# Kernel optimization log

Hardware: AMD Instinct MI355X
Metric: run time of the kernel (lower is better)

## Reference

```python
import jax, jax.numpy as jnp
import numpy as np

B, C, H, W = 16, 768, 32, 32
HEADS = 12
EPS = 1e-5


def _make_rel_index(h, w):
    coords = np.stack(np.meshgrid(np.arange(h), np.arange(w), indexing='ij'))  # [2,h,w]
    cf = coords.reshape(2, -1)                      # [2,N]
    rel = cf[:, :, None] - cf[:, None, :]           # [2,N,N]
    rel = rel.transpose(1, 2, 0).copy()             # [N,N,2]
    rel[:, :, 0] += h - 1
    rel[:, :, 1] += w - 1
    rel[:, :, 0] *= 2 * w - 1
    return jnp.asarray(rel.sum(-1), dtype=jnp.int32)  # [N,N]


def setup_inputs() -> dict:
    key = jax.random.key(0)
    ks = jax.random.split(key, 8)
    s = 0.02
    return {
        'x': jax.random.normal(ks[0], (B, C, H, W), jnp.float32),
        'rpb_table': jax.random.normal(ks[1], ((2 * H - 1) * (2 * W - 1), HEADS), jnp.float32) * s,
        'g1': jnp.ones((C,), jnp.float32),
        'b1': jnp.zeros((C,), jnp.float32),
        'q_w': jax.random.normal(ks[2], (C, C), jnp.float32) * s,
        'q_b': jnp.zeros((C,), jnp.float32),
        'kv_w': jax.random.normal(ks[3], (2 * C, C), jnp.float32) * s,
        'kv_b': jnp.zeros((2 * C,), jnp.float32),
        'proj_w': jax.random.normal(ks[4], (C, C), jnp.float32) * s,
        'proj_b': jnp.zeros((C,), jnp.float32),
        'g2': jnp.ones((C,), jnp.float32),
        'b2': jnp.zeros((C,), jnp.float32),
        'fc1_w': jax.random.normal(ks[5], (4 * C, C), jnp.float32) * s,
        'fc1_b': jnp.zeros((4 * C,), jnp.float32),
        'fc2_w': jax.random.normal(ks[6], (C, 4 * C), jnp.float32) * s,
        'fc2_b': jnp.zeros((C,), jnp.float32),
        'rel_index': _make_rel_index(H, W),
    }


def _ln(t, g, b):
    m = t.mean(-1, keepdims=True)
    v = ((t - m) ** 2).mean(-1, keepdims=True)
    return (t - m) * jax.lax.rsqrt(v + EPS) * g + b


def reference(x, rpb_table, g1, b1, q_w, q_b, kv_w, kv_b, proj_w, proj_b,
              g2, b2, fc1_w, fc1_b, fc2_w, fc2_b, rel_index):
    b, c, h, w = x.shape
    n = h * w
    heads = rpb_table.shape[1]
    hd = c // heads
    scale = hd ** -0.5

    xt = x.reshape(b, c, n).transpose(0, 2, 1)  # [B,N,C]

    # --- attention branch ---
    xn = _ln(xt, g1, b1)
    q = (xn @ q_w.T + q_b).reshape(b, n, heads, hd).transpose(0, 2, 1, 3)  # [B,h,N,d]
    kv = (xn @ kv_w.T + kv_b).reshape(b, n, 2, heads, hd)
    k = kv[:, :, 0].transpose(0, 2, 1, 3)  # [B,h,N,d]
    v = kv[:, :, 1].transpose(0, 2, 1, 3)  # [B,h,N,d]
    attn = jnp.einsum('bhnd,bhmd->bhnm', q, k) * scale  # [B,h,N,N]
    bias = rpb_table[rel_index].transpose(2, 0, 1)      # [h,N,N]
    attn = jax.nn.softmax(attn + bias[None], axis=-1)
    o = jnp.einsum('bhnm,bhmd->bhnd', attn, v).transpose(0, 2, 1, 3).reshape(b, n, c)
    o = o @ proj_w.T + proj_b
    xt = xt + o

    # --- mlp branch ---
    xn = _ln(xt, g2, b2)
    h1 = jax.nn.gelu(xn @ fc1_w.T + fc1_b, approximate=False)
    xt = xt + (h1 @ fc2_w.T + fc2_b)

    return xt.transpose(0, 2, 1).reshape(b, c, h, w)
```

## Files before the change

### kernel.cpp

```cpp
#include <hip/hip_runtime.h>
#include <hip/hip_bf16.h>
#include <math.h>

typedef unsigned short u16;
typedef unsigned int u32;
typedef float f32x4 __attribute__((ext_vector_type(4)));
typedef short bf16x8 __attribute__((ext_vector_type(8)));
typedef unsigned short us4 __attribute__((ext_vector_type(4)));
typedef int i32x4 __attribute__((ext_vector_type(4)));

struct alignas(16) F4 { float v[4]; };
template <int N> struct Tag { static constexpr int v = N; };

static constexpr int Bb = 16;
static constexpr int Cc = 768;
static constexpr int Nn = 1024;
static constexpr int NH = 12;
static constexpr int HD = 64;
static constexpr float LOG2E = 1.4426950408889634f;

static __device__ __forceinline__ u16 f2bf(float f) {
  union { float f; unsigned u; } v; v.f = f;
  unsigned u = v.u;
  u += 0x7fffu + ((u >> 16) & 1u);
  return (u16)(u >> 16);
}
static __device__ __forceinline__ float bf2f(u16 x) {
  union { unsigned u; float f; } v; v.u = ((unsigned)x) << 16; return v.f;
}
static __device__ __forceinline__ void gload16(const u16* g, u16* l) {
  __builtin_amdgcn_global_load_lds((const __attribute__((address_space(1))) u32*)g,
                                   (__attribute__((address_space(3))) u32*)l, 16, 0, 0);
}
static __device__ __forceinline__ float gelu_f(float v) {
  float z = v * 0.70710678118654752f;
  float az = fabsf(z);
  float t = __builtin_amdgcn_rcpf(1.f + 0.3275911f * az);
  float poly = t * (0.254829592f + t * (-0.284496736f + t * (1.421413741f +
               t * (-1.453152027f + t * 1.061405429f))));
  float e = __builtin_amdgcn_exp2f(-az * az * LOG2E);
  float erfv = 1.f - poly * e;
  erfv = (z < 0.f) ? -erfv : erfv;
  return 0.5f * v * (1.f + erfv);
}
static __device__ __forceinline__ us4 pack4(const float* s) {
  us4 r;
  r[0] = f2bf(s[0]); r[1] = f2bf(s[1]); r[2] = f2bf(s[2]); r[3] = f2bf(s[3]);
  return r;
}

__global__ __launch_bounds__(256) void k_pre_all(const float* __restrict__ q_w,
    const float* __restrict__ kv_w, const float* __restrict__ proj_w,
    const float* __restrict__ fc1_w, const float* __restrict__ fc2_w,
    const float* __restrict__ q_b, const float* __restrict__ kv_b,
    u16* __restrict__ wqkv, u16* __restrict__ wproj, u16* __restrict__ wfc1,
    u16* __restrict__ wfc2, float* __restrict__ bqkv,
    const float* __restrict__ x, u16* __restrict__ xt,
    const float* __restrict__ rpb, const int* __restrict__ rel,
    u16* __restrict__ bias2) {
  const int bid = blockIdx.x, tid = threadIdx.x;
  if (bid < 6913) {
    int i4 = bid * 256 + tid;
    if (i4 >= 1769664) return;
    int i = i4 * 4;
    if (i < 589824) {
      f32x4 sv = *(const f32x4*)&q_w[i];
      *(us4*)&wqkv[i] = pack4((const float*)&sv);
    } else if (i < 1769472) {
      f32x4 sv = *(const f32x4*)&kv_w[i - 589824];
      *(us4*)&wqkv[i] = pack4((const float*)&sv);
    } else if (i < 2359296) {
      f32x4 sv = *(const f32x4*)&proj_w[i - 1769472];
      *(us4*)&wproj[i - 1769472] = pack4((const float*)&sv);
    } else if (i < 4718592) {
      f32x4 sv = *(const f32x4*)&fc1_w[i - 2359296];
      *(us4*)&wfc1[i - 2359296] = pack4((const float*)&sv);
    } else if (i < 7077888) {
      f32x4 sv = *(const f32x4*)&fc2_w[i - 4718592];
      *(us4*)&wfc2[i - 4718592] = pack4((const float*)&sv);
    } else if (i < 7078656) {
      f32x4 sv;
      if (i - 7077888 < 768) sv = *(const f32x4*)&q_b[i - 7077888];
      else                   sv = *(const f32x4*)&kv_b[i - 7078656];
      *(f32x4*)&bqkv[i - 7077888] = sv;
    } else {
      f32x4 sv = *(const f32x4*)&kv_b[i - 7078656];
      *(f32x4*)&bqkv[i - 7077888] = sv;
    }
  } else if (bid < 19201) {
    __shared__ float tile[32][33];
    int j = bid - 6913;
    int n0 = (j & 31) * 32, c0 = ((j >> 5) % 24) * 32, b = j / 768;
    int tx = tid & 31, ty = tid >> 5;
    const float* xp = x + (size_t)b * Cc * Nn;
    #pragma unroll
    for (int i = 0; i < 32; i += 8)
      tile[ty + i][tx] = xp[(size_t)(c0 + ty + i) * Nn + n0 + tx];
    __syncthreads();
    u16* xtp = xt + (size_t)b * Nn * Cc;
    #pragma unroll
    for (int i = 0; i < 32; i += 8)
      xtp[(size_t)(n0 + ty + i) * Cc + c0 + tx] = f2bf(tile[tx][ty + i]);
  } else {
    int idx = (bid - 19201) * 256 + tid;
    int kg = idx & 255, q = (idx >> 8) & 1023, h = idx >> 18;
    int k = kg * 4;
    i32x4 rv = *(const i32x4*)&rel[(size_t)q * Nn + k];
    us4 ov;
    ov[0] = f2bf(rpb[rv[0] * NH + h] * LOG2E);
    ov[1] = f2bf(rpb[rv[1] * NH + h] * LOG2E);
    ov[2] = f2bf(rpb[rv[2] * NH + h] * LOG2E);
    ov[3] = f2bf(rpb[rv[3] * NH + h] * LOG2E);
    *(us4*)&bias2[((size_t)h * Nn + q) * Nn + k] = ov;
  }
}

__global__ __launch_bounds__(256) void k_layernorm(const u16* __restrict__ in,
    const float* __restrict__ gam, const float* __restrict__ bet,
    u16* __restrict__ out) {
  int wave = threadIdx.x >> 6, lane = threadIdx.x & 63;
  int row = blockIdx.x * 4 + wave;
  const u16* p = in + (size_t)row * Cc;
  float v[12]; float s = 0.f;
  #pragma unroll
  for (int i = 0; i < 6; i++) {
    u32 pr = *(const u32*)&p[2 * (lane + i * 64)];
    v[2 * i]     = bf2f((u16)(pr & 0xffff));
    v[2 * i + 1] = bf2f((u16)(pr >> 16));
    s += v[2 * i] + v[2 * i + 1];
  }
  #pragma unroll
  for (int m = 32; m >= 1; m >>= 1) s += __shfl_xor(s, m);
  float mean = s * (1.f / 768.f);
  float q = 0.f;
  #pragma unroll
  for (int i = 0; i < 12; i++) { float d = v[i] - mean; q += d * d; }
  #pragma unroll
  for (int m = 32; m >= 1; m >>= 1) q += __shfl_xor(q, m);
  float rstd = rsqrtf(q * (1.f / 768.f) + 1e-5f);
  u16* o = out + (size_t)row * Cc;
  #pragma unroll
  for (int i = 0; i < 6; i++) {
    int j = 2 * (lane + i * 64);
    u16 lo = f2bf((v[2 * i]     - mean) * rstd * gam[j]     + bet[j]);
    u16 hi = f2bf((v[2 * i + 1] - mean) * rstd * gam[j + 1] + bet[j + 1]);
    *(u32*)&o[j] = (u32)lo | ((u32)hi << 16);
  }
}

struct GemmArgs {
  const u16* A; const u16* W; const float* bias;
  int M, N, K;
  const u16* resBf;
  float* outF;
  u16* outBf;
  u16 *q, *k, *v;
};

template <int EPI>
__global__ __launch_bounds__(512, 2) void k_gemm(GemmArgs p) {
  extern __shared__ f32x4 smv[];
  u16* lA = (u16*)smv;
  u16* lB = (u16*)smv + 2 * 256 * 64;
  const int tid = threadIdx.x;
  const int wave = tid >> 6, lane = tid & 63;
  const int l15 = lane & 15, g = lane >> 4, h7 = l15 & 7;
  const int wr = wave >> 2, wc = wave & 3;
  const int rl = tid >> 3, cc8 = tid & 7;
  const int nwg = gridDim.x * gridDim.y;
  const int wg = blockIdx.y * gridDim.x + blockIdx.x;
  const int swz = (wg & 7) * (nwg >> 3) + (wg >> 3);
  const int bn = (swz % gridDim.x) * 256, bm = (swz / gridDim.x) * 256;
  const int K = p.K;

  f32x4 acc[8][4];
  #pragma unroll
  for (int i = 0; i < 8; i++)
    #pragma unroll
    for (int j = 0; j < 4; j++) acc[i][j] = (f32x4){0.f, 0.f, 0.f, 0.f};

  const u16* Ab = p.A + (size_t)bm * K;
  const u16* Wb = p.W + (size_t)bn * K;
  const int csw = (cc8 ^ (rl & 7)) * 8;

  auto stageA = [&](int buf, int k0, int half) {
    int r0 = half * 64 + rl, r1 = r0 + 128;
    gload16(Ab + (size_t)r0 * K + k0 + csw, &lA[buf * 16384 + r0 * 64 + cc8 * 8]);
    gload16(Ab + (size_t)r1 * K + k0 + csw, &lA[buf * 16384 + r1 * 64 + cc8 * 8]);
  };
  auto stageB = [&](int buf, int k0, int half) {
    int r0 = ((rl >> 5) << 6) + half * 32 + (rl & 31), r1 = r0 + 128;
    gload16(Wb + (size_t)r0 * K + k0 + csw, &lB[buf * 16384 + r0 * 64 + cc8 * 8]);
    gload16(Wb + (size_t)r1 * K + k0 + csw, &lB[buf * 16384 + r1 * 64 + cc8 * 8]);
  };

  bf16x8 a[4][2], bq[4][2];
  auto rdA = [&](int buf, int mt, int kk) {
    int row = wr * 128 + mt * 16 + l15;
    return *(const bf16x8*)&lA[buf * 16384 + row * 64 + (((kk << 2) + g) ^ h7) * 8];
  };
  auto rdB = [&](int buf, int nt, int kk) {
    int row = wc * 64 + nt * 16 + l15;
    return *(const bf16x8*)&lB[buf * 16384 + row * 64 + (((kk << 2) + g) ^ h7) * 8];
  };
  auto MF = [&](auto MBt, auto NBt) {
    constexpr int MB = decltype(MBt)::v, NB = decltype(NBt)::v;
    __builtin_amdgcn_s_setprio(1);
    #pragma unroll
    for (int kk = 0; kk < 2; kk++)
      #pragma unroll
      for (int mi = 0; mi < 4; mi++)
        #pragma unroll
        for (int ni = 0; ni < 2; ni++)
          acc[MB + mi][NB + ni] = __builtin_amdgcn_mfma_f32_16x16x32_bf16(
              a[mi][kk], bq[NB + ni][kk], acc[MB + mi][NB + ni], 0, 0, 0);
    __builtin_amdgcn_s_setprio(0);
  };

  stageA(0, 0, 0); stageB(0, 0, 0); stageB(0, 0, 1); stageA(0, 0, 1);
  stageA(1, 64, 0);
  asm volatile("s_waitcnt vmcnt(6)" ::: "memory");
  __builtin_amdgcn_s_barrier();

  auto TILE = [&](int t, auto tag) {
    constexpr int TAIL = decltype(tag)::v;
    const int buf = t & 1, nb = buf ^ 1;
    const int k1 = (t + 1) * 64;
    #pragma unroll
    for (int mi = 0; mi < 4; mi++) { a[mi][0] = rdA(buf, mi, 0); a[mi][1] = rdA(buf, mi, 1); }
    #pragma unroll
    for (int ni = 0; ni < 2; ni++) { bq[ni][0] = rdB(buf, ni, 0); bq[ni][1] = rdB(buf, ni, 1); }
    if constexpr (TAIL < 2) {
      stageB(nb, k1, 0);
      asm volatile("s_waitcnt vmcnt(6)" ::: "memory");
    } else {
      asm volatile("s_waitcnt vmcnt(2)" ::: "memory");
    }
    __builtin_amdgcn_s_barrier();
    __builtin_amdgcn_sched_barrier(0);
    MF(Tag<0>{}, Tag<0>{});
    #pragma unroll
    for (int ni = 0; ni < 2; ni++) { bq[2 + ni][0] = rdB(buf, 2 + ni, 0); bq[2 + ni][1] = rdB(buf, 2 + ni, 1); }
    if constexpr (TAIL < 2) {
      stageB(nb, k1, 1);
      asm volatile("s_waitcnt vmcnt(6)" ::: "memory");
    } else {
      asm volatile("s_waitcnt vmcnt(0)" ::: "memory");
    }
    __builtin_amdgcn_s_barrier();
    __builtin_amdgcn_sched_barrier(0);
    MF(Tag<0>{}, Tag<2>{});
    #pragma unroll
    for (int mi = 0; mi < 4; mi++) { a[mi][0] = rdA(buf, 4 + mi, 0); a[mi][1] = rdA(buf, 4 + mi, 1); }
    if constexpr (TAIL < 2) stageA(nb, k1, 1);
    __builtin_amdgcn_s_barrier();
    __builtin_amdgcn_sched_barrier(0);
    MF(Tag<4>{}, Tag<2>{});
    if constexpr (TAIL == 0) {
      stageA(buf, k1 + 64, 0);
      asm volatile("s_waitcnt vmcnt(6)" ::: "memory");
    } else if constexpr (TAIL == 1) {
      asm volatile("s_waitcnt vmcnt(4)" ::: "memory");
    }
    __builtin_amdgcn_s_barrier();
    __builtin_amdgcn_sched_barrier(0);
    MF(Tag<4>{}, Tag<0>{});
  };

  const int NT = K >> 6;
  for (int t = 0; t < NT - 2; ++t) TILE(t, Tag<0>{});
  TILE(NT - 2, Tag<1>{});
  TILE(NT - 1, Tag<2>{});

  #pragma unroll
  for (int mt = 0; mt < 8; mt++) {
    int rowb = bm + wr * 128 + mt * 16 + g * 4;
    #pragma unroll
    for (int nt = 0; nt < 4; nt++) {
      int col = bn + wc * 64 + nt * 16 + l15;
      float bias = p.bias[col];
      if constexpr (EPI == 0) {
        #pragma unroll
        for (int r = 0; r < 4; r++) {
          int grow = rowb + r;
          int bb = grow >> 10, nnq = grow & 1023;
          float val = acc[mt][nt][r] + bias;
          if (col < 768) {
            int head = col >> 6, d = col & 63;
            p.q[(((size_t)bb * NH + head) * Nn + nnq) * HD + d] = f2bf(val * (0.125f * LOG2E));
          } else {
            int j2 = col - 768;
            if (j2 < 768) {
              int head = j2 >> 6, d = j2 & 63;
              p.k[(((size_t)bb * NH + head) * Nn + nnq) * HD + d] = f2bf(val);
            } else {
              int j3 = j2 - 768;
              int head = j3 >> 6, d = j3 & 63;
              p.v[(((size_t)bb * NH + head) * HD + d) * Nn + nnq] = f2bf(val);
            }
          }
        }
      } else if constexpr (EPI == 1) {
        #pragma unroll
        for (int r = 0; r < 4; r++) {
          size_t idx = (size_t)(rowb + r) * p.N + col;
          p.outBf[idx] = f2bf(acc[mt][nt][r] + bias + bf2f(p.resBf[idx]));
        }
      } else if constexpr (EPI == 2) {
        #pragma unroll
        for (int r = 0; r < 4; r++) {
          float val = acc[mt][nt][r] + bias;
          p.outBf[(size_t)(rowb + r) * p.N + col] = f2bf(gelu_f(val));
        }
      } else {
        int bb = rowb >> 10, n0 = rowb & 1023;
        F4 ov;
        #pragma unroll
        for (int r = 0; r < 4; r++)
          ov.v[r] = acc[mt][nt][r] + bias + bf2f(p.resBf[(size_t)(rowb + r) * Cc + col]);
        *(F4*)&p.outF[((size_t)bb * Cc + col) * Nn + n0] = ov;
      }
    }
  }
}

__global__ __launch_bounds__(512, 4) void k_attn(const u16* __restrict__ qt,
    const u16* __restrict__ kt_, const u16* __restrict__ vtt,
    const u16* __restrict__ bias2, u16* __restrict__ o) {
  __shared__ __align__(16) u16 lK[3][64 * 64];
  __shared__ __align__(16) u16 lV[3][64 * 64];
  __shared__ __align__(16) u16 lP[8][16 * 64];
  const int tid = threadIdx.x, wave = tid >> 6, lane = tid & 63;
  const int l15 = lane & 15, g = lane >> 4;
  const int i_ = blockIdx.x;
  const int slot = i_ >> 3;
  const int hx = (i_ & 7) * 12 + (slot >> 4);
  const int b = slot & 15, h = hx >> 3;
  const int q0 = (hx & 7) * 128 + wave * 16;
  const size_t bh  = ((size_t)b * NH + h) * Nn * HD;
  const size_t bhT = ((size_t)b * NH + h) * HD * Nn;
  const u16* biasH = bias2 + (size_t)h * Nn * Nn;
  u16* myP = &lP[wave][0];
  const float THR = 8.f * LOG2E;
  const int sRow = tid >> 3, sCol = tid & 7;
  const int h7 = l15 & 7;

  bf16x8 qa0, qa1;
  {
    const u16* qp = qt + bh + (size_t)(q0 + l15) * HD + g * 8;
    qa0 = *(const bf16x8*)qp;
    qa1 = *(const bf16x8*)(qp + 32);
  }
  bf16x8 ones;
  #pragma unroll
  for (int i = 0; i < 8; i++) ones[i] = (short)0x3F80;

  f32x4 ao[4];
  f32x4 al;
  float mr = -1e30f;
  #pragma unroll
  for (int d = 0; d < 4; d++) ao[d] = (f32x4){0.f, 0.f, 0.f, 0.f};
  al = (f32x4){0.f, 0.f, 0.f, 0.f};

  auto issueKV = [&](int kt0, int buf) {
    int cs = (sCol ^ (sRow & 7)) << 3;
    gload16(kt_ + bh + (size_t)(kt0 + sRow) * HD + cs, &lK[buf][sRow * 64 + sCol * 8]);
    gload16(vtt + bhT + (size_t)sRow * Nn + kt0 + cs, &lV[buf][sRow * 64 + sCol * 8]);
  };

  issueKV(0, 0);
  issueKV(64, 1);
  int buf = 0, nbuf = 2;
  for (int t = 0; t < 16; ++t) {
    if (t < 15) asm volatile("s_waitcnt vmcnt(2) lgkmcnt(0)" ::: "memory");
    else        asm volatile("s_waitcnt vmcnt(0) lgkmcnt(0)" ::: "memory");
    __builtin_amdgcn_s_barrier();
    __builtin_amdgcn_sched_barrier(0);

    us4 bvv[4];
    #pragma unroll
    for (int nt = 0; nt < 4; nt++)
      bvv[nt] = *(const us4*)(biasH + (size_t)(q0 + l15) * Nn + t * 64 + nt * 16 + g * 4);
    __builtin_amdgcn_sched_barrier(0);
    if (t < 14) issueKV((t + 2) * 64, nbuf);
    __builtin_amdgcn_sched_barrier(0);

    f32x4 s[4];
    __builtin_amdgcn_s_setprio(1);
    #pragma unroll
    for (int nt = 0; nt < 4; nt++) {
      const int row = nt * 16 + l15;
      bf16x8 kb0 = *(const bf16x8*)&lK[buf][row * 64 + ((g ^ h7) << 3)];
      bf16x8 kb1 = *(const bf16x8*)&lK[buf][row * 64 + (((g + 4) ^ h7) << 3)];
      s[nt] = __builtin_amdgcn_mfma_f32_16x16x32_bf16(kb0, qa0,
                (f32x4){0.f, 0.f, 0.f, 0.f}, 0, 0, 0);
      s[nt] = __builtin_amdgcn_mfma_f32_16x16x32_bf16(kb1, qa1, s[nt], 0, 0, 0);
    }
    __builtin_amdgcn_s_setprio(0);

    #pragma unroll
    for (int nt = 0; nt < 4; nt++) {
      #pragma unroll
      for (int r = 0; r < 4; r++) s[nt][r] += bf2f(bvv[nt][r]);
    }
    float pm = fmaxf(fmaxf(s[0][0], s[0][1]), fmaxf(s[0][2], s[0][3]));
    #pragma unroll
    for (int nt = 1; nt < 4; nt++)
      pm = fmaxf(pm, fmaxf(fmaxf(s[nt][0], s[nt][1]), fmaxf(s[nt][2], s[nt][3])));
    pm = fmaxf(pm, __shfl_xor(pm, 16));
    pm = fmaxf(pm, __shfl_xor(pm, 32));
    if (__any(pm > mr + THR)) {
      float mnew = fmaxf(mr, pm);
      float fac = __builtin_amdgcn_exp2f(mr - mnew);
      mr = mnew;
      f32x4 facO;
      #pragma unroll
      for (int r = 0; r < 4; r++) facO[r] = __shfl(fac, g * 4 + r);
      #pragma unroll
      for (int d = 0; d < 4; d++) ao[d] *= facO;
      al *= facO;
    }
    #pragma unroll
    for (int nt = 0; nt < 4; nt++) {
      #pragma unroll
      for (int r = 0; r < 4; r++)
        s[nt][r] = __builtin_amdgcn_exp2f(s[nt][r] - mr);
    }
    #pragma unroll
    for (int nt = 0; nt < 4; nt++) {
      u32 w0, w1;
      asm("v_cvt_pk_bf16_f32 %0, %1, %2" : "=v"(w0) : "v"(s[nt][0]), "v"(s[nt][1]));
      asm("v_cvt_pk_bf16_f32 %0, %1, %2" : "=v"(w1) : "v"(s[nt][2]), "v"(s[nt][3]));
      int cbase = (((2 * nt + (g >> 1)) ^ h7) << 3) + (g & 1) * 4;
      *(u32*)&myP[l15 * 64 + cbase]     = w0;
      *(u32*)&myP[l15 * 64 + cbase + 2] = w1;
    }
    __builtin_amdgcn_s_setprio(1);
    #pragma unroll
    for (int kc = 0; kc < 2; kc++) {
      bf16x8 pa = *(const bf16x8*)&myP[l15 * 64 + (((4 * kc + g) ^ h7) << 3)];
      al = __builtin_amdgcn_mfma_f32_16x16x32_bf16(pa, ones, al, 0, 0, 0);
      #pragma unroll
      for (int d = 0; d < 4; d++) {
        const int rv = d * 16 + l15;
        bf16x8 vb = *(const bf16x8*)&lV[buf][rv * 64 + (((kc * 4 + g) ^ h7) << 3)];
        ao[d] = __builtin_amdgcn_mfma_f32_16x16x32_bf16(pa, vb, ao[d], 0, 0, 0);
      }
    }
    __builtin_amdgcn_s_setprio(0);
    buf = (buf == 2) ? 0 : buf + 1;
    nbuf = (nbuf == 2) ? 0 : nbuf + 1;
  }
  f32x4 linv;
  #pragma unroll
  for (int r = 0; r < 4; r++) linv[r] = __builtin_amdgcn_rcpf(al[r]);
  #pragma unroll
  for (int r = 0; r < 4; r++) {
    int qg = q0 + g * 4 + r;
    u16* op = o + ((size_t)b * Nn + qg) * Cc + h * HD;
    #pragma unroll
    for (int d = 0; d < 4; d++)
      op[d * 16 + l15] = f2bf(ao[d][r] * linv[r]);
  }
}

extern "C" void kernel_launch(void* const* d_in, const int* in_sizes, int n_in,
                              void* d_out, int out_size, void* d_ws, size_t ws_size,
                              hipStream_t stream) {
  const float* x      = (const float*)d_in[0];
  const float* rpb    = (const float*)d_in[1];
  const float* g1     = (const float*)d_in[2];
  const float* b1v    = (const float*)d_in[3];
  const float* q_w    = (const float*)d_in[4];
  const float* q_b    = (const float*)d_in[5];
  const float* kv_w   = (const float*)d_in[6];
  const float* kv_b   = (const float*)d_in[7];
  const float* proj_w = (const float*)d_in[8];
  const float* proj_b = (const float*)d_in[9];
  const float* g2     = (const float*)d_in[10];
  const float* b2v    = (const float*)d_in[11];
  const float* fc1_w  = (const float*)d_in[12];
  const float* fc1_b  = (const float*)d_in[13];
  const float* fc2_w  = (const float*)d_in[14];
  const float* fc2_b  = (const float*)d_in[15];
  const int*   rel    = (const int*)d_in[16];
  float* out = (float*)d_out;

  char* ws = (char*)d_ws;
  size_t off = 0;
  auto alloc = [&](size_t bytes) -> void* {
    void* p = ws + off;
    off += (bytes + 255) & ~(size_t)255;
    return p;
  };
  u16*   wqkv  = (u16*)alloc((size_t)2304 * 768 * 2);
  u16*   wproj = (u16*)alloc((size_t)768 * 768 * 2);
  u16*   wfc1  = (u16*)alloc((size_t)3072 * 768 * 2);
  u16*   wfc2  = (u16*)alloc((size_t)768 * 3072 * 2);
  float* bqkv  = (float*)alloc((size_t)2304 * 4);
  u16*   xt    = (u16*)alloc((size_t)16384 * 768 * 2);
  u16*   xt2   = (u16*)alloc((size_t)16384 * 768 * 2);
  u16*   xn    = (u16*)alloc((size_t)16384 * 768 * 2);
  u16*   qb_   = (u16*)alloc((size_t)Bb * NH * Nn * HD * 2);
  u16*   kb_   = (u16*)alloc((size_t)Bb * NH * Nn * HD * 2);
  u16*   vb_   = (u16*)alloc((size_t)Bb * NH * Nn * HD * 2);
  u16*   ob_   = (u16*)alloc((size_t)16384 * 768 * 2);
  u16*   h1    = qb_;
  u16*   bias2 = xt2;

  hipFuncSetAttribute((const void*)k_gemm<0>, hipFuncAttributeMaxDynamicSharedMemorySize, 131072);
  hipFuncSetAttribute((const void*)k_gemm<1>, hipFuncAttributeMaxDynamicSharedMemorySize, 131072);
  hipFuncSetAttribute((const void*)k_gemm<2>, hipFuncAttributeMaxDynamicSharedMemorySize, 131072);
  hipFuncSetAttribute((const void*)k_gemm<3>, hipFuncAttributeMaxDynamicSharedMemorySize, 131072);

  k_pre_all<<<31489, 256, 0, stream>>>(q_w, kv_w, proj_w, fc1_w, fc2_w, q_b, kv_b,
                                       wqkv, wproj, wfc1, wfc2, bqkv,
                                       x, xt, rpb, rel, bias2);

  k_layernorm<<<4096, 256, 0, stream>>>(xt, g1, b1v, xn);

  GemmArgs ga = {};
  ga.A = xn; ga.W = wqkv; ga.bias = bqkv; ga.M = 16384; ga.N = 2304; ga.K = 768;
  ga.q = qb_; ga.k = kb_; ga.v = vb_;
  k_gemm<0><<<dim3(9, 64), 512, 131072, stream>>>(ga);

  k_attn<<<1536, 512, 0, stream>>>(qb_, kb_, vb_, bias2, ob_);

  GemmArgs gp = {};
  gp.A = ob_; gp.W = wproj; gp.bias = proj_b; gp.M = 16384; gp.N = 768; gp.K = 768;
  gp.resBf = xt; gp.outBf = xt2;
  k_gemm<1><<<dim3(3, 64), 512, 131072, stream>>>(gp);

  k_layernorm<<<4096, 256, 0, stream>>>(xt2, g2, b2v, xn);

  GemmArgs gf1 = {};
  gf1.A = xn; gf1.W = wfc1; gf1.bias = fc1_b; gf1.M = 16384; gf1.N = 3072; gf1.K = 768;
  gf1.outBf = h1;
  k_gemm<2><<<dim3(12, 64), 512, 131072, stream>>>(gf1);

  GemmArgs gf2 = {};
  gf2.A = h1; gf2.W = wfc2; gf2.bias = fc2_b; gf2.M = 16384; gf2.N = 768; gf2.K = 3072;
  gf2.resBf = xt2; gf2.outF = out;
  k_gemm<3><<<dim3(3, 64), 512, 131072, stream>>>(gf2);
}
```

Before: 491.4 us.

## Use smaller 128x128 tile GEMM kernel for N=768 projection and fc2

Adds a new GEMM kernel with 128x128 tiles, 256 threads and static shared memory, and uses it for the proj and fc2 GEMMs whose N=768 gave only 192 workgroups with the large-tile kernel. The goal is to raise the workgroup count to 768 so all compute units get work and waves are better balanced. The new kernel has no multi-stage pipelining: it does a single-buffered K loop with synchronizations around direct loads, so per-tile efficiency may be lower and the smaller tiles give less data reuse.

```diff
diff --git a/kernel.cpp b/kernel.cpp
--- a/kernel.cpp
+++ b/kernel.cpp
@@ -300,17 +300,77 @@
             }
           }
         }
-      } else if constexpr (EPI == 1) {
-        #pragma unroll
-        for (int r = 0; r < 4; r++) {
-          size_t idx = (size_t)(rowb + r) * p.N + col;
-          p.outBf[idx] = f2bf(acc[mt][nt][r] + bias + bf2f(p.resBf[idx]));
-        }
       } else if constexpr (EPI == 2) {
         #pragma unroll
         for (int r = 0; r < 4; r++) {
           float val = acc[mt][nt][r] + bias;
           p.outBf[(size_t)(rowb + r) * p.N + col] = f2bf(gelu_f(val));
+        }
+      }
+    }
+  }
+}
+
+template <int EPI>
+__global__ __launch_bounds__(256) void k_gemm128(GemmArgs p) {
+  __shared__ __align__(16) u16 lA[128 * 32];
+  __shared__ __align__(16) u16 lB[128 * 32];
+  const int tid = threadIdx.x;
+  const int wave = tid >> 6, lane = tid & 63;
+  const int l15 = lane & 15, g = lane >> 4;
+  const int wrow = wave >> 1, wcol = wave & 1;
+  const int nwg = gridDim.x * gridDim.y;
+  const int wg = blockIdx.y * gridDim.x + blockIdx.x;
+  const int swz = (wg & 7) * (nwg >> 3) + (wg >> 3);
+  const int bn = (swz % gridDim.x) * 128, bm = (swz / gridDim.x) * 128;
+  const int K = p.K;
+  f32x4 acc[4][4];
+  #pragma unroll
+  for (int i = 0; i < 4; i++)
+    #pragma unroll
+    for (int j = 0; j < 4; j++) acc[i][j] = (f32x4){0.f, 0.f, 0.f, 0.f};
+
+  const u16* Ab = p.A + (size_t)bm * K;
+  const u16* Wb = p.W + (size_t)bn * K;
+  const int c0 = tid, c1 = tid + 256;
+  const int r0 = c0 >> 2, k80 = (c0 & 3) * 8;
+  const int r1 = c1 >> 2, k81 = (c1 & 3) * 8;
+
+  for (int kt = 0; kt < K; kt += 32) {
+    __syncthreads();
+    gload16(Ab + (size_t)r0 * K + kt + k80, &lA[c0 * 8]);
+    gload16(Ab + (size_t)r1 * K + kt + k81, &lA[c1 * 8]);
+    gload16(Wb + (size_t)r0 * K + kt + k80, &lB[c0 * 8]);
+    gload16(Wb + (size_t)r1 * K + kt + k81, &lB[c1 * 8]);
+    __syncthreads();
+    bf16x8 af[4], bfr[4];
+    #pragma unroll
+    for (int mt = 0; mt < 4; mt++)
+      af[mt] = *(const bf16x8*)&lA[(wrow * 64 + mt * 16 + l15) * 32 + g * 8];
+    #pragma unroll
+    for (int nt = 0; nt < 4; nt++)
+      bfr[nt] = *(const bf16x8*)&lB[(wcol * 64 + nt * 16 + l15) * 32 + g * 8];
+    __builtin_amdgcn_s_setprio(1);
+    #pragma unroll
+    for (int mt = 0; mt < 4; mt++)
+      #pragma unroll
+      for (int nt = 0; nt < 4; nt++)
+        acc[mt][nt] = __builtin_amdgcn_mfma_f32_16x16x32_bf16(af[mt], bfr[nt], acc[mt][nt], 0, 0, 0);
+    __builtin_amdgcn_s_setprio(0);
+  }
+
+  #pragma unroll
+  for (int mt = 0; mt < 4; mt++) {
+    int rowb = bm + wrow * 64 + mt * 16 + g * 4;
+    #pragma unroll
+    for (int nt = 0; nt < 4; nt++) {
+      int col = bn + wcol * 64 + nt * 16 + l15;
+      float bias = p.bias[col];
+      if constexpr (EPI == 1) {
+        #pragma unroll
+        for (int r = 0; r < 4; r++) {
+          size_t idx = (size_t)(rowb + r) * p.N + col;
+          p.outBf[idx] = f2bf(acc[mt][nt][r] + bias + bf2f(p.resBf[idx]));
         }
       } else {
         int bb = rowb >> 10, n0 = rowb & 1023;
@@ -509,9 +569,7 @@
   u16*   bias2 = xt2;
 
   hipFuncSetAttribute((const void*)k_gemm<0>, hipFuncAttributeMaxDynamicSharedMemorySize, 131072);
-  hipFuncSetAttribute((const void*)k_gemm<1>, hipFuncAttributeMaxDynamicSharedMemorySize, 131072);
   hipFuncSetAttribute((const void*)k_gemm<2>, hipFuncAttributeMaxDynamicSharedMemorySize, 131072);
-  hipFuncSetAttribute((const void*)k_gemm<3>, hipFuncAttributeMaxDynamicSharedMemorySize, 131072);
 
   k_pre_all<<<31489, 256, 0, stream>>>(q_w, kv_w, proj_w, fc1_w, fc2_w, q_b, kv_b,
                                        wqkv, wproj, wfc1, wfc2, bqkv,
@@ -529,7 +587,7 @@
   GemmArgs gp = {};
   gp.A = ob_; gp.W = wproj; gp.bias = proj_b; gp.M = 16384; gp.N = 768; gp.K = 768;
   gp.resBf = xt; gp.outBf = xt2;
-  k_gemm<1><<<dim3(3, 64), 512, 131072, stream>>>(gp);
+  k_gemm128<1><<<dim3(6, 128), 256, 0, stream>>>(gp);
 
   k_layernorm<<<4096, 256, 0, stream>>>(xt2, g2, b2v, xn);
 
@@ -541,5 +599,5 @@
   GemmArgs gf2 = {};
   gf2.A = h1; gf2.W = wfc2; gf2.bias = fc2_b; gf2.M = 16384; gf2.N = 768; gf2.K = 3072;
   gf2.resBf = xt2; gf2.outF = out;
-  k_gemm<3><<<dim3(3, 64), 512, 131072, stream>>>(gf2);
-}
+  k_gemm128<3><<<dim3(6, 128), 256, 0, stream>>>(gf2);
+}
```

Measured after the change: 500.4 us. No clear change (+1.8%).
